# Performance work log

Measured on AMD Instinct MI355X. Metric: run time of the kernel, lower is better.

Reference implementation:

```python
import jax, jax.numpy as jnp
import numpy as np

IMC = 256
EPS = 1e-6
BN_EPS = 1e-5
GRID = (69.12, 79.36)      # (depth, width) in meters
OFF = (0.0, -39.68, 0.0)   # (xoff, yoff, zoff)
RES = 0.64
ZMIN, ZMAX = -3.0, 2.76
SCALES = [0.25, 0.125, 0.0625, 0.03125, 0.015625]


def make_corners():
    # replicates make_grid(): corner lattice in lidar coords, shape [nz, nx, ny, 3]
    nx = int(round(GRID[0] / RES)) + 1   # 109
    ny = int(round(GRID[1] / RES)) + 1   # 125
    nz = int(round((ZMAX - ZMIN) / RES)) + 1  # 10
    xc = RES * np.arange(nx) + OFF[0]
    yc = GRID[1] - RES * np.arange(ny) + OFF[1]
    zc = ZMAX - RES * np.arange(nz)
    xx, yy = np.meshgrid(xc, yc, indexing='ij')
    base = np.stack([xx, yy, np.full_like(xx, OFF[2])], axis=-1)  # [nx,ny,3]
    zoffs = np.stack([np.zeros(nz), np.zeros(nz), zc], axis=-1)   # [nz,3]
    corners = base[None] + zoffs[:, None, None, :]
    return jnp.asarray(corners, jnp.float32)


def grid_sample(img, grid):
    # img [B,C,H,W]; grid [B,P,N,2] xy in [-1,1]; bilinear, zero padding, align_corners=False
    B, C, H, W = img.shape
    x = (grid[..., 0] + 1.0) * (W * 0.5) - 0.5
    y = (grid[..., 1] + 1.0) * (H * 0.5) - 0.5
    x0f = jnp.floor(x); y0f = jnp.floor(y)
    wx = (x - x0f).reshape(B, 1, -1)
    wy = (y - y0f).reshape(B, 1, -1)
    x0 = x0f.astype(jnp.int32); y0 = y0f.astype(jnp.int32)
    flat = img.reshape(B, C, H * W)
    def g(xi, yi):
        ok = ((xi >= 0) & (xi < W) & (yi >= 0) & (yi < H)).reshape(B, 1, -1)
        idx = (jnp.clip(yi, 0, H - 1) * W + jnp.clip(xi, 0, W - 1)).reshape(B, 1, -1)
        return jnp.take_along_axis(flat, idx, axis=2) * ok
    v00 = g(x0, y0); v01 = g(x0 + 1, y0); v10 = g(x0, y0 + 1); v11 = g(x0 + 1, y0 + 1)
    out = (v00 * (1 - wx) + v01 * wx) * (1 - wy) + (v10 * (1 - wx) + v11 * wx) * wy
    return out.reshape(B, C, grid.shape[1], grid.shape[2])


def oft(feats, calib, corners, scale, w, b):
    B, C, Hf, Wf = feats.shape
    # perspective projection of grid corners into the image plane
    hom = jnp.einsum('bij,zdwj->bzdwi', calib[:, :, :3], corners) + calib[:, None, None, None, :, 3]
    xy = hom[..., :2] / hom[..., 2:3]                      # [B,nz,nx,ny,2]
    img_size = jnp.array([Wf, Hf], jnp.float32) / scale
    nc = jnp.clip(2.0 * xy / img_size - 1.0, -1.0, 1.0)
    mn = jnp.minimum(nc[:, :-1, :-1, :-1], nc[:, :-1, 1:, :-1])
    mx = jnp.maximum(nc[:, 1:, 1:, 1:], nc[:, 1:, :-1, 1:])
    bbox = jnp.concatenate([mn, mx], axis=-1)              # [B,Zc,Dc,Wc,4]
    _, Zc, Dc, Wc, _ = bbox.shape
    bbox = bbox.reshape(B, Zc, Dc * Wc, 4)
    area = ((bbox[..., 2] - bbox[..., 0]) * (bbox[..., 3] - bbox[..., 1])
            * (Hf * Wf * 0.25) + EPS)[:, None]             # [B,1,Zc,N]
    visible = (area > EPS).astype(feats.dtype)
    ii = jnp.cumsum(jnp.cumsum(feats, axis=-1), axis=-2)   # integral image
    tl = grid_sample(ii, jnp.stack([bbox[..., 0], bbox[..., 1]], -1))
    br = grid_sample(ii, jnp.stack([bbox[..., 2], bbox[..., 3]], -1))
    tr = grid_sample(ii, jnp.stack([bbox[..., 2], bbox[..., 1]], -1))
    bl = grid_sample(ii, jnp.stack([bbox[..., 0], bbox[..., 3]], -1))
    vox = (tl + br - tr - bl) / area * visible             # [B,C,Zc,N]
    vox = vox.transpose(0, 3, 1, 2).reshape(B * Dc * Wc, C * Zc)
    ortho = jax.nn.relu(vox @ w.T + b).reshape(B, Dc, Wc, -1)
    return ortho.transpose(0, 3, 2, 1)                     # [B,imc,Wc,Dc]


def attention(x, aw, ab):
    s = jax.nn.sigmoid(x.mean(axis=(2, 3)) @ aw.T + ab)
    return x * s[:, :, None, None]


def conv3x3(x, w, stride):
    return jax.lax.conv_general_dilated(x, w, (stride, stride), ((1, 1), (1, 1)),
                                        dimension_numbers=('NCHW', 'OIHW', 'NCHW'))


def bn(x, g, b, m, v):
    scale = g / jnp.sqrt(v + BN_EPS)
    return (x - m[None, :, None, None]) * scale[None, :, None, None] + b[None, :, None, None]


def make_calib(B):
    K = np.array([[560.0, 0.0, 640.0], [0.0, 560.0, 192.0], [0.0, 0.0, 1.0]])
    Rt = np.array([[0.0, -1.0, 0.0, 0.05],   # lidar(x fwd, y left, z up) -> cam(x right, y down, z fwd)
                   [0.0, 0.0, -1.0, -0.30],
                   [1.0, 0.0, 0.0, 0.27]])
    P = K @ Rt
    return jnp.asarray(np.tile(P[None], (B, 1, 1)), jnp.float32)


def setup_inputs() -> dict:
    key = jax.random.key(0)
    ks = jax.random.split(key, 16)
    B = 1
    shapes = [(B, IMC, 96, 320), (B, IMC, 48, 160), (B, IMC, 24, 80), (B, IMC, 12, 40), (B, IMC, 6, 20)]
    feats = [jax.random.normal(ks[i], s, jnp.float32) * 0.1 for i, s in enumerate(shapes)]
    HC = 9 * IMC  # height_channels = int((2.76-(-3))/0.64 * 256) = 2304
    inp = {
        'feats04': feats[0], 'feats08': feats[1], 'feats16': feats[2],
        'feats32': feats[3], 'feats64': feats[4],
        'calib': make_calib(B),
        'oft_w': jax.random.normal(ks[5], (5, IMC, HC), jnp.float32) * 0.02,
        'oft_b': jax.random.normal(ks[6], (5, IMC), jnp.float32) * 0.02,
        'att_w': jax.random.normal(ks[7], (IMC, IMC), jnp.float32) * 0.05,
        'att_b': jnp.zeros((IMC,), jnp.float32),
        'conv1_w': jax.random.normal(ks[8], (IMC, IMC * 5, 3, 3), jnp.float32) * 0.02,
        'bn1_g': 1.0 + 0.1 * jax.random.normal(ks[9], (IMC,), jnp.float32),
        'bn1_b': 0.05 * jax.random.normal(ks[10], (IMC,), jnp.float32),
        'bn1_m': 0.05 * jax.random.normal(ks[11], (IMC,), jnp.float32),
        'bn1_v': jax.random.uniform(ks[12], (IMC,), jnp.float32, 0.5, 1.5),
        'conv2_w': jax.random.normal(ks[13], (IMC, IMC, 3, 3), jnp.float32) * 0.02,
        'bn2_g': 1.0 + 0.1 * jax.random.normal(ks[14], (IMC,), jnp.float32),
        'bn2_b': jnp.zeros((IMC,), jnp.float32),
        'bn2_m': jnp.zeros((IMC,), jnp.float32),
        'bn2_v': jax.random.uniform(ks[15], (IMC,), jnp.float32, 0.5, 1.5),
    }
    return inp


def reference(feats04, feats08, feats16, feats32, feats64, calib,
              oft_w, oft_b, att_w, att_b,
              conv1_w, bn1_g, bn1_b, bn1_m, bn1_v,
              conv2_w, bn2_g, bn2_b, bn2_m, bn2_v):
    corners = make_corners()
    feats = [feats04, feats08, feats16, feats32, feats64]
    orthos = [attention(oft(f, calib, corners, s, oft_w[i], oft_b[i]), att_w, att_b)
              for i, (f, s) in enumerate(zip(feats, SCALES))]
    x = jnp.concatenate(orthos, axis=1)            # [B, 5*imc, 124, 108]
    x = jax.nn.relu(bn(conv3x3(x, conv1_w, 2), bn1_g, bn1_b, bn1_m, bn1_v))
    x = jax.nn.relu(bn(conv3x3(x, conv2_w, 1), bn2_g, bn2_b, bn2_m, bn2_v))
    return x                                       # [B, imc, 62, 54]
```

## Files before the change

### kernel.cpp

```cpp
#include <hip/hip_runtime.h>

typedef __attribute__((ext_vector_type(8))) short short8;
typedef __attribute__((ext_vector_type(4))) float float4v;
typedef __attribute__((ext_vector_type(4))) int int4v;
typedef __attribute__((ext_vector_type(4))) unsigned short ushort4v;

#define NBOX 13392
#define ZC 9
#define KOFT 2304
#define NPIX 3348
#define NBLK0 105
#define NBLKC 27
#define TILEK 4096
#define NBSTRIDE 294912
#define VOXSZ 30965760

__device__ __forceinline__ unsigned short f2bf(float f) {
  union { float f; unsigned int i; } v; v.f = f;
  unsigned int r = v.i + 0x7FFFu + ((v.i >> 16) & 1u);
  return (unsigned short)(r >> 16);
}
__device__ __forceinline__ float bf2f(unsigned short u) {
  union { unsigned int i; float f; } v; v.i = ((unsigned int)u) << 16; return v.f;
}
__device__ __forceinline__ float i2f(int i) {
  union { int i; float f; } v; v.i = i; return v.f;
}

__device__ __forceinline__ const int* uniform_ptr(const int* p) {
  unsigned lo = (unsigned)(uintptr_t)p;
  unsigned hi = (unsigned)((uintptr_t)p >> 32);
  lo = (unsigned)__builtin_amdgcn_readfirstlane((int)lo);
  hi = (unsigned)__builtin_amdgcn_readfirstlane((int)hi);
  return (const int*)(((uintptr_t)hi << 32) | (uintptr_t)lo);
}

__device__ __forceinline__ void async16(const unsigned short* g, unsigned short* l) {
  __builtin_amdgcn_global_load_lds(
      (const __attribute__((address_space(1))) unsigned int*)g,
      (__attribute__((address_space(3))) unsigned int*)l, 16, 0, 0);
}

__global__ void k_alpha_beta(const float* __restrict__ oft_b,
                             const float* __restrict__ g1, const float* __restrict__ b1,
                             const float* __restrict__ m1, const float* __restrict__ v1,
                             const float* __restrict__ g2, const float* __restrict__ b2,
                             const float* __restrict__ m2, const float* __restrict__ v2,
                             float* __restrict__ ALPHA, float* __restrict__ BETA,
                             float* __restrict__ MEANS, unsigned short* __restrict__ ZPAGE) {
  int g = blockIdx.x, c = threadIdx.x;
  float al, be;
  if (g < 5) { al = 1.f; be = oft_b[g * 256 + c]; MEANS[g * 256 + c] = 0.f; }
  else {
    const float* gg = (g == 5) ? g1 : g2;
    const float* bb = (g == 5) ? b1 : b2;
    const float* mm = (g == 5) ? m1 : m2;
    const float* vv = (g == 5) ? v1 : v2;
    al = gg[c] / sqrtf(vv[c] + 1e-5f);
    be = bb[c] - mm[c] * al;
  }
  ALPHA[g * 256 + c] = al; BETA[g * 256 + c] = be;
  if (g == 0) ZPAGE[c] = 0;
}

__global__ void k_wpermT(const float* __restrict__ w, unsigned short* __restrict__ wp) {
  int idx = blockIdx.x * 256 + threadIdx.x;
  int sc = idx / 589824;
  int r  = idx % 589824;
  int j   = r & 7;
  int row = (r >> 3) & 127;
  int kc  = (r >> 10) & 3;
  int cs  = r >> 12;
  int cb  = cs / 72, s = cs % 72;
  int oc = cb * 128 + row;
  int k  = s * 32 + kc * 8 + j;
  int z = k >> 8, c = k & 255;
  wp[idx] = f2bf(w[((size_t)sc * 256 + oc) * 2304 + c * 9 + z]);
}

__global__ void k_wperm1T(const float* __restrict__ w, const float* __restrict__ satt,
                          unsigned short* __restrict__ wp) {
  int idx = blockIdx.x * 256 + threadIdx.x;
  int j   = idx & 7;
  int row = (idx >> 3) & 127;
  int kc  = (idx >> 10) & 3;
  int rest = idx >> 12;
  int s = rest % 40; rest /= 40;
  int r = rest % 9;  int cb = rest / 9;
  int oc = cb * 128 + row;
  int ic = s * 32 + kc * 8 + j;
  wp[idx] = f2bf(w[(size_t)oc * 11520 + ic * 9 + r] * satt[ic]);
}

__global__ void k_wperm2T(const float* __restrict__ w, unsigned short* __restrict__ wp) {
  int idx = blockIdx.x * 256 + threadIdx.x;
  int j   = idx & 7;
  int row = (idx >> 3) & 127;
  int kc  = (idx >> 10) & 3;
  int rest = idx >> 12;
  int s = rest % 8; rest /= 8;
  int r = rest % 9; int cb = rest / 9;
  int oc = cb * 128 + row;
  int ic = s * 32 + kc * 8 + j;
  wp[idx] = f2bf(w[(size_t)oc * 2304 + ic * 9 + r]);
}

__global__ void k_taps(const float* __restrict__ calib, int* __restrict__ taps,
                       int Hf, int Wf, float areaScale) {
  int idx = blockIdx.x * 256 + threadIdx.x;
  if (idx >= ZC * NBOX) return;
  int z = idx / NBOX, n = idx % NBOX;
  int d = n / 124, wj = n % 124;
  float P[12];
#pragma unroll
  for (int i = 0; i < 12; ++i) P[i] = calib[i];
  auto proj = [&](int k, int i, int j, float& nxo, float& nyo) {
    float X = 0.64f * (float)i;
    float Y = 39.68f - 0.64f * (float)j;
    float Z = 2.76f - 0.64f * (float)k;
    float hx = P[0] * X + P[1] * Y + P[2]  * Z + P[3];
    float hy = P[4] * X + P[5] * Y + P[6]  * Z + P[7];
    float hz = P[8] * X + P[9] * Y + P[10] * Z + P[11];
    float px = hx / hz, py = hy / hz;
    nxo = 2.f * px / 1280.f - 1.f; nxo = fminf(fmaxf(nxo, -1.f), 1.f);
    nyo = 2.f * py / 384.f  - 1.f; nyo = fminf(fmaxf(nyo, -1.f), 1.f);
  };
  float ax, ay, bx, by, cx, cy, dx, dy;
  proj(z,     d,     wj,     ax, ay);
  proj(z,     d + 1, wj,     bx, by);
  proj(z + 1, d + 1, wj + 1, cx, cy);
  proj(z + 1, d,     wj + 1, dx, dy);
  float x0 = fminf(ax, bx), y0 = fminf(ay, by);
  float x1 = fmaxf(cx, dx), y1 = fmaxf(cy, dy);
  float rawA = (x1 - x0) * (y1 - y0) * areaScale;
  int* ob = taps + (size_t)idx * 32;
  if (!(rawA > 0.f)) { ob[0] = 0; return; }
  float inv = 1.f / (rawA + 1e-6f);

  float u0 = (x0 + 1.f) * ((float)Wf * 0.5f) - 0.5f;
  float u1 = (x1 + 1.f) * ((float)Wf * 0.5f) - 0.5f;
  float fu0 = floorf(u0), fu1 = floorf(u1);
  int cx0 = (int)fu0, cx1 = (int)fu1;
  float wx0 = u0 - fu0, wx1 = u1 - fu1;
  int xs[4]; float xw[4];
  xs[0] = cx0; xs[1] = cx0 + 1; xs[2] = cx1; xs[3] = cx1 + 1;
  xw[0] = (1.f - wx0) * inv; xw[1] = wx0 * inv;
  xw[2] = -(1.f - wx1) * inv; xw[3] = -wx1 * inv;
  int dcx = cx1 - cx0;
  if (dcx == 0)      { xw[0] += xw[2]; xw[1] += xw[3]; xw[2] = 0.f; xw[3] = 0.f; }
  else if (dcx == 1) { xw[1] += xw[2]; xw[2] = xw[3]; xs[2] = xs[3]; xw[3] = 0.f; }
#pragma unroll
  for (int j = 0; j < 4; ++j) {
    if (xs[j] < 0 || xs[j] >= Wf) xw[j] = 0.f;
    xs[j] = min(max(xs[j], 0), Wf - 1);
  }
#define CSWX(a, b) { if (xw[a] == 0.f && xw[b] != 0.f) { \
    float tw = xw[a]; xw[a] = xw[b]; xw[b] = tw; \
    int ts = xs[a]; xs[a] = xs[b]; xs[b] = ts; } }
  CSWX(0, 1) CSWX(2, 3) CSWX(0, 2) CSWX(1, 3) CSWX(1, 2)
#undef CSWX
  int nx = (xw[0] != 0.f) + (xw[1] != 0.f) + (xw[2] != 0.f) + (xw[3] != 0.f);

  float v0 = (y0 + 1.f) * ((float)Hf * 0.5f) - 0.5f;
  float v1 = (y1 + 1.f) * ((float)Hf * 0.5f) - 0.5f;
  float fv0 = floorf(v0), fv1 = floorf(v1);
  int ry0 = (int)fv0, ry1 = (int)fv1;
  float wy0 = v0 - fv0, wy1 = v1 - fv1;
  int ys[4]; float yw[4];
  ys[0] = ry0; ys[1] = ry0 + 1; ys[2] = ry1; ys[3] = ry1 + 1;
  yw[0] = 1.f - wy0; yw[1] = wy0; yw[2] = -(1.f - wy1); yw[3] = -wy1;
  int dcy = ry1 - ry0;
  if (dcy == 0)      { yw[0] += yw[2]; yw[1] += yw[3]; yw[2] = 0.f; yw[3] = 0.f; }
  else if (dcy == 1) { yw[1] += yw[2]; yw[2] = yw[3]; ys[2] = ys[3]; yw[3] = 0.f; }
#pragma unroll
  for (int j = 0; j < 4; ++j) {
    if (ys[j] < 0 || ys[j] >= Hf) yw[j] = 0.f;
    ys[j] = min(max(ys[j], 0), Hf - 1);
  }
#define CSWY(a, b) { if (yw[a] == 0.f && yw[b] != 0.f) { \
    float tw = yw[a]; yw[a] = yw[b]; yw[b] = tw; \
    int ts = ys[a]; ys[a] = ys[b]; ys[b] = ts; } }
  CSWY(0, 1) CSWY(2, 3) CSWY(0, 2) CSWY(1, 3) CSWY(1, 2)
#undef CSWY
  int ny = (yw[0] != 0.f) + (yw[1] != 0.f) + (yw[2] != 0.f) + (yw[3] != 0.f);

  if (nx == 0 || ny == 0) { ob[0] = 0; return; }

  int off[16]; float w[16];
#pragma unroll
  for (int r = 0; r < 4; ++r)
#pragma unroll
    for (int c = 0; c < 4; ++c) {
      off[r * 4 + c] = (ys[r] * Wf + xs[c]) * 1024;
      w[r * 4 + c] = yw[r] * xw[c];
    }
  off[0] |= (nx << 25) | (ny << 28);
  int4v* obv = (int4v*)ob;
#pragma unroll
  for (int i = 0; i < 4; ++i)
    obv[i] = (int4v){off[4 * i], off[4 * i + 1], off[4 * i + 2], off[4 * i + 3]};
  float4v* wb = (float4v*)obv;
#pragma unroll
  for (int i = 0; i < 4; ++i)
    wb[4 + i] = (float4v){w[4 * i], w[4 * i + 1], w[4 * i + 2], w[4 * i + 3]};
}

__global__ void k_transpose_all(const float* __restrict__ f0, const float* __restrict__ f1,
                                const float* __restrict__ f2, const float* __restrict__ f3,
                                const float* __restrict__ f4, float* __restrict__ II) {
  int b = blockIdx.x;
  int sc, cx;
  if (b < 480)      { sc = 0; cx = b; }
  else if (b < 600) { sc = 1; cx = b - 480; }
  else if (b < 630) { sc = 2; cx = b - 600; }
  else if (b < 638) { sc = 3; cx = b - 630; }
  else              { sc = 4; cx = b - 638; }
  const int Ss[5] = {30720, 7680, 1920, 480, 120};
  const size_t IIof[5] = {0, 7864320, 9830400, 10321920, 10444800};
  const float* srcs[5] = {f0, f1, f2, f3, f4};
  int S = Ss[sc];
  const float* src = srcs[sc];
  float* dst = II + IIof[sc];
  __shared__ float tile[64][65];
  int t = threadIdx.x;
  int wave = t >> 6, lane = t & 63;
  int s0 = cx * 64, c0 = blockIdx.y * 64;
#pragma unroll
  for (int i = 0; i < 16; ++i) {
    int c_l = wave * 16 + i;
    if (s0 + lane < S) tile[c_l][lane] = src[(size_t)(c0 + c_l) * S + s0 + lane];
  }
  __syncthreads();
#pragma unroll
  for (int i = 0; i < 16; ++i) {
    int s_l = wave * 16 + i;
    if (s0 + s_l < S) dst[(size_t)(s0 + s_l) * 256 + c0 + lane] = tile[lane][s_l];
  }
}

__global__ void k_cumw_all(float* __restrict__ II) {
  int b = blockIdx.x;
  int sc, h;
  if (b < 96)       { sc = 0; h = b; }
  else if (b < 144) { sc = 1; h = b - 96; }
  else if (b < 168) { sc = 2; h = b - 144; }
  else if (b < 180) { sc = 3; h = b - 168; }
  else              { sc = 4; h = b - 180; }
  const int Wfs[5] = {320, 160, 80, 40, 20};
  const size_t IIof[5] = {0, 7864320, 9830400, 10321920, 10444800};
  int Wf = Wfs[sc];
  float* p = II + IIof[sc] + (size_t)h * Wf * 256 + threadIdx.x;
  float acc = 0.f;
#pragma unroll 4
  for (int w = 0; w < Wf; ++w) { acc += p[(size_t)w * 256]; p[(size_t)w * 256] = acc; }
}

__global__ void k_cumh_all(float* __restrict__ II) {
  int b = blockIdx.x;
  int sc, w;
  if (b < 320)      { sc = 0; w = b; }
  else if (b < 480) { sc = 1; w = b - 320; }
  else if (b < 560) { sc = 2; w = b - 480; }
  else if (b < 600) { sc = 3; w = b - 560; }
  else              { sc = 4; w = b - 600; }
  const int Wfs[5] = {320, 160, 80, 40, 20};
  const int Hfs[5] = {96, 48, 24, 12, 6};
  const size_t IIof[5] = {0, 7864320, 9830400, 10321920, 10444800};
  int Hf = Hfs[sc];
  size_t stride = (size_t)Wfs[sc] * 256;
  float* p = II + IIof[sc] + (size_t)w * 256 + threadIdx.x;
  float acc = 0.f;
#pragma unroll 4
  for (int h = 0; h < Hf; ++h) { acc += p[h * stride]; p[h * stride] = acc; }
}

__global__ __launch_bounds__(512) void k_sample(const float* __restrict__ ii,
                                                const int* __restrict__ taps,
                                                unsigned short* __restrict__ voxT) {
  __shared__ unsigned short st[3][8][66][4];
  int t = threadIdx.x;
  int wave = t >> 6, lane = t & 63;
  int n = blockIdx.x * 8 + wave;
  int zg = blockIdx.y * 3;
  const char* iib = (const char*)ii + (lane << 4);
#pragma unroll
  for (int dz = 0; dz < 3; ++dz) {
    int z = zg + dz;
    const int* tb = uniform_ptr(taps + (size_t)(z * NBOX + n) * 32);
    int o_[16];
#pragma unroll
    for (int i = 0; i < 16; ++i) o_[i] = tb[i];
    unsigned h = (unsigned)o_[0];
    int nx = (h >> 25) & 7;
    int ny = (h >> 28) & 7;
    o_[0] = (int)(h & 0x01FFFFFFu);
    ushort4v o;
    if (ny == 0) {
      o[0] = 0; o[1] = 0; o[2] = 0; o[3] = 0;
    } else {
      float w_[16];
#pragma unroll
      for (int i = 0; i < 16; ++i) w_[i] = i2f(tb[16 + i]);
      float4v a0 = {0.f, 0.f, 0.f, 0.f}, a1 = a0;
#define TAP(i, acc) { float4v t_ = *(const float4v*)(iib + (size_t)(unsigned)o_[i]); acc += t_ * w_[i]; }
      TAP(0, a0)
      if (nx > 1) TAP(1, a1)
      if (nx > 2) TAP(2, a0)
      if (nx > 3) TAP(3, a1)
      if (ny > 1) {
        TAP(4, a0)
        if (nx > 1) TAP(5, a1)
        if (nx > 2) TAP(6, a0)
        if (nx > 3) TAP(7, a1)
      }
      if (ny > 2) {
        TAP(8, a0)
        if (nx > 1) TAP(9, a1)
        if (nx > 2) TAP(10, a0)
        if (nx > 3) TAP(11, a1)
      }
      if (ny > 3) {
        TAP(12, a0)
        if (nx > 1) TAP(13, a1)
        if (nx > 2) TAP(14, a0)
        if (nx > 3) TAP(15, a1)
      }
#undef TAP
      float4v acc = a0 + a1;
#pragma unroll
      for (int j = 0; j < 4; ++j) o[j] = f2bf(acc[j]);
    }
    *(ushort4v*)&st[dz][wave][lane][0] = o;
  }
  __syncthreads();
  int nb = (blockIdx.x * 8) >> 7;
  int r0 = (blockIdx.x * 8) & 127;
  unsigned short* outb = voxT + (size_t)nb * NBSTRIDE + (size_t)r0 * 32;
  int lane32 = t & 31;
  int row = lane32 >> 2, kc = lane32 & 3;
  int kcS = kc ^ ((row >> 1) & 3);
#pragma unroll
  for (int p = 0; p < 2; ++p) {
    int q = p * 16 + (t >> 5);
    if (q < 24) {
      int zq = q >> 3;
      int si = q & 7;
      short8 v = *(const short8*)&st[zq][row][si * 8 + kc * 2][0];
      *(short8*)(outb + (size_t)(zg + zq) * 32768 + (size_t)si * 4096
                 + (size_t)(row * 32 + kcS * 8)) = v;
    }
  }
}

__global__ __launch_bounds__(256) void k_gemmT_all(
    const unsigned short* __restrict__ AT, const unsigned short* __restrict__ BT,
    const float* __restrict__ beta, unsigned short* __restrict__ xbuf, int s0) {
  __shared__ unsigned short ls[8704];
  unsigned short* lsA = ls;
  unsigned short* lsB = ls + 4096;
  int t = threadIdx.x;
  int lane = t & 63, wave = t >> 6;
  int l15 = lane & 15, quad = lane >> 4;
  int nb = blockIdx.x, cb = blockIdx.y;
  int slab = blockIdx.z, sc = s0 + slab;
  int wrow = (wave >> 1) * 64, wcol = (wave & 1) * 64;
  int quadS = quad ^ ((l15 >> 1) & 3);

  const unsigned short* ga = AT + (size_t)slab * VOXSZ + (size_t)nb * NBSTRIDE + t * 8;
  const unsigned short* gb = BT + (size_t)sc * 589824 + (size_t)cb * NBSTRIDE + t * 8;
  unsigned short* ldA = lsA + t * 8;
  unsigned short* ldB = lsB + t * 8;

  float4v acc[4][4];
#pragma unroll
  for (int mi = 0; mi < 4; ++mi)
#pragma unroll
    for (int ni = 0; ni < 4; ++ni) acc[mi][ni] = (float4v){0.f, 0.f, 0.f, 0.f};

  for (int s = 0; s < 72; ++s) {
    async16(ga, ldA);
    async16(ga + 2048, ldA + 2048);
    async16(gb, ldB);
    async16(gb + 2048, ldB + 2048);
    ga += TILEK; gb += TILEK;
    __syncthreads();
    short8 af[4], bf[4];
    const short8* pA = (const short8*)lsA;
    const short8* pB = (const short8*)lsB;
#pragma unroll
    for (int mi = 0; mi < 4; ++mi) af[mi] = pA[(wrow + mi * 16 + l15) * 4 + quadS];
#pragma unroll
    for (int ni = 0; ni < 4; ++ni) bf[ni] = pB[quad * 128 + wcol + ni * 16 + l15];
#pragma unroll
    for (int mi = 0; mi < 4; ++mi)
#pragma unroll
      for (int ni = 0; ni < 4; ++ni)
        acc[mi][ni] = __builtin_amdgcn_mfma_f32_16x16x32_bf16(af[mi], bf[ni], acc[mi][ni], 0, 0, 0);
    __syncthreads();
  }

  float bval[4];
#pragma unroll
  for (int ni = 0; ni < 4; ++ni)
    bval[ni] = beta[sc * 256 + cb * 128 + wcol + ni * 16 + l15];
#pragma unroll
  for (int ph = 0; ph < 2; ++ph) {
    if (wrow == ph * 64) {
#pragma unroll
      for (int mi = 0; mi < 4; ++mi)
#pragma unroll
        for (int ni = 0; ni < 4; ++ni)
#pragma unroll
          for (int j = 0; j < 4; ++j) {
            int row = mi * 16 + quad * 4 + j;
            int col = wcol + ni * 16 + l15;
            float v = acc[mi][ni][j] + bval[ni];
            ls[row * 136 + col] = f2bf(v > 0.f ? v : 0.f);
          }
    }
    __syncthreads();
#pragma unroll
    for (int it = 0; it < 4; ++it) {
      int idx = it * 256 + t;
      int row = idx >> 4, ch = idx & 15;
      int nn = nb * 128 + ph * 64 + row;
      if (nn < NBOX) {
        short8 v = *(const short8*)&ls[row * 136 + ch * 8];
        *(short8*)(xbuf + (size_t)nn * 1280 + sc * 256 + cb * 128 + ch * 8) = v;
      }
    }
    __syncthreads();
  }
}

__global__ __launch_bounds__(256) void k_gemmT(
    const unsigned short* __restrict__ AT, const unsigned short* __restrict__ BT,
    float* __restrict__ part) {
  __shared__ unsigned short lsA[4096];
  __shared__ unsigned short lsB[4096];
  int t = threadIdx.x;
  int lane = t & 63, wave = t >> 6;
  int l15 = lane & 15, quad = lane >> 4;
  int nb = blockIdx.x, cb = blockIdx.y, ks = blockIdx.z;
  int wrow = (wave >> 1) * 64, wcol = (wave & 1) * 64;
  int quadS = quad ^ ((l15 >> 1) & 3);

  const unsigned short* ga = AT + (size_t)nb * NBSTRIDE + (size_t)ks * 18 * TILEK + t * 8;
  const unsigned short* gb = BT + (size_t)cb * NBSTRIDE + (size_t)ks * 18 * TILEK + t * 8;
  unsigned short* ldA = lsA + t * 8;
  unsigned short* ldB = lsB + t * 8;

  float4v acc[4][4];
#pragma unroll
  for (int mi = 0; mi < 4; ++mi)
#pragma unroll
    for (int ni = 0; ni < 4; ++ni) acc[mi][ni] = (float4v){0.f, 0.f, 0.f, 0.f};

  for (int s = 0; s < 18; ++s) {
    async16(ga, ldA);
    async16(ga + 2048, ldA + 2048);
    async16(gb, ldB);
    async16(gb + 2048, ldB + 2048);
    ga += TILEK; gb += TILEK;
    __syncthreads();
    short8 af[4], bf[4];
    const short8* pA = (const short8*)lsA;
    const short8* pB = (const short8*)lsB;
#pragma unroll
    for (int mi = 0; mi < 4; ++mi) af[mi] = pA[(wrow + mi * 16 + l15) * 4 + quadS];
#pragma unroll
    for (int ni = 0; ni < 4; ++ni) bf[ni] = pB[quad * 128 + wcol + ni * 16 + l15];
#pragma unroll
    for (int mi = 0; mi < 4; ++mi)
#pragma unroll
      for (int ni = 0; ni < 4; ++ni)
        acc[mi][ni] = __builtin_amdgcn_mfma_f32_16x16x32_bf16(af[mi], bf[ni], acc[mi][ni], 0, 0, 0);
    __syncthreads();
  }

#pragma unroll
  for (int mi = 0; mi < 4; ++mi) {
    int nb0 = nb * 128 + wrow + mi * 16 + quad * 4;
#pragma unroll
    for (int j = 0; j < 4; ++j) {
      int nn = nb0 + j;
      if (nn < NBOX) {
#pragma unroll
        for (int ni = 0; ni < 4; ++ni) {
          int oc = cb * 128 + wcol + ni * 16 + l15;
          part[((size_t)ks * NBOX + nn) * 256 + oc] = acc[mi][ni][j];
        }
      }
    }
  }
}

__global__ void k_redoft(const float* __restrict__ part, const float* __restrict__ beta,
                         unsigned short* __restrict__ xbuf, int choff) {
  int n = blockIdx.x, oc = threadIdx.x;
  float v = part[(size_t)n * 256 + oc]
          + part[((size_t)NBOX + n) * 256 + oc]
          + part[((size_t)2 * NBOX + n) * 256 + oc]
          + part[((size_t)3 * NBOX + n) * 256 + oc];
  v += beta[oc];
  v = v > 0.f ? v : 0.f;
  xbuf[(size_t)n * 1280 + choff + oc] = f2bf(v);
}

template <int MODE>
__global__ __launch_bounds__(256) void k_gemmS(
    const unsigned short* __restrict__ A, const unsigned short* __restrict__ BT,
    float* __restrict__ part, const unsigned short* __restrict__ zpage) {
  constexpr int KIC   = (MODE == 1) ? 1280 : 256;
  constexpr int STEPS = KIC / 32;
  __shared__ unsigned short lsA[4096];
  __shared__ unsigned short lsB[4096];
  int t = threadIdx.x;
  int lane = t & 63, wave = t >> 6;
  int l15 = lane & 15, quad = lane >> 4;
  int n0 = blockIdx.x * 128, oc0 = blockIdx.y * 128;
  int r = blockIdx.z;
  int wrow = (wave >> 1) * 64, wcol = (wave & 1) * 64;
  int srow = t & 127, skc = t >> 7;

  int p = n0 + srow;
  int oy = p / 54, ox = p - oy * 54;
  int ky = r / 3, kx = r - ky * 3;
  bool valid; int sp;
  if (MODE == 1) {
    int ih = 2 * oy + ky - 1, iw = 2 * ox + kx - 1;
    valid = (p < NPIX) && ((unsigned)ih < 124u) && ((unsigned)iw < 108u);
    sp = iw * 124 + ih;
  } else {
    int ih = oy + ky - 1, iw = ox + kx - 1;
    valid = (p < NPIX) && ((unsigned)ih < 62u) && ((unsigned)iw < 54u);
    sp = ih * 54 + iw;
  }
  const unsigned short* ga = valid ? (A + (size_t)sp * KIC + skc * 8) : zpage;
  int astep = valid ? 32 : 0;
  const unsigned short* gb = BT + ((size_t)(blockIdx.y * 9 + r) * STEPS) * TILEK + t * 8;
  unsigned short* ldA = lsA + t * 8;
  unsigned short* ldB = lsB + t * 8;

  float4v acc[4][4];
#pragma unroll
  for (int mi = 0; mi < 4; ++mi)
#pragma unroll
    for (int ni = 0; ni < 4; ++ni) acc[mi][ni] = (float4v){0.f, 0.f, 0.f, 0.f};

  for (int s = 0; s < STEPS; ++s) {
    async16(ga, ldA);
    async16(ga + 16, ldA + 2048);
    async16(gb, ldB);
    async16(gb + 2048, ldB + 2048);
    ga += astep; gb += TILEK;
    __syncthreads();
    short8 af[4], bf[4];
    const short8* pA = (const short8*)lsA;
    const short8* pB = (const short8*)lsB;
#pragma unroll
    for (int mi = 0; mi < 4; ++mi) af[mi] = pA[quad * 128 + wrow + mi * 16 + l15];
#pragma unroll
    for (int ni = 0; ni < 4; ++ni) bf[ni] = pB[quad * 128 + wcol + ni * 16 + l15];
#pragma unroll
    for (int mi = 0; mi < 4; ++mi)
#pragma unroll
      for (int ni = 0; ni < 4; ++ni)
        acc[mi][ni] = __builtin_amdgcn_mfma_f32_16x16x32_bf16(af[mi], bf[ni], acc[mi][ni], 0, 0, 0);
    __syncthreads();
  }

#pragma unroll
  for (int mi = 0; mi < 4; ++mi) {
    int nb0 = n0 + wrow + mi * 16 + quad * 4;
#pragma unroll
    for (int j = 0; j < 4; ++j) {
      int nn = nb0 + j;
      if (nn < NPIX) {
#pragma unroll
        for (int ni = 0; ni < 4; ++ni) {
          int oc = oc0 + wcol + ni * 16 + l15;
          part[((size_t)r * NPIX + nn) * 256 + oc] = acc[mi][ni][j];
        }
      }
    }
  }
}

template <bool F32OUT>
__global__ void k_redconv(const float* __restrict__ part, const float* __restrict__ alpha,
                          const float* __restrict__ beta, void* __restrict__ outv) {
  int p = blockIdx.x, oc = threadIdx.x;
  float v = 0.f;
#pragma unroll
  for (int r = 0; r < 9; ++r) v += part[((size_t)r * NPIX + p) * 256 + oc];
  v = v * alpha[oc] + beta[oc];
  v = v > 0.f ? v : 0.f;
  if (F32OUT) ((float*)outv)[(size_t)oc * NPIX + p] = v;
  else ((unsigned short*)outv)[(size_t)p * 256 + oc] = f2bf(v);
}

__global__ void k_means2(const unsigned short* __restrict__ x, float* __restrict__ means) {
  int tid = threadIdx.x;
  if (tid >= 160) return;
  int c0 = tid * 8;
  int r0 = blockIdx.x * 64;
  float part[8] = {0.f, 0.f, 0.f, 0.f, 0.f, 0.f, 0.f, 0.f};
  for (int i = 0; i < 64; ++i) {
    int row = r0 + i;
    if (row < NBOX) {
      short8 v = *(const short8*)(x + (size_t)row * 1280 + c0);
#pragma unroll
      for (int j = 0; j < 8; ++j) part[j] += bf2f((unsigned short)v[j]);
    }
  }
#pragma unroll
  for (int j = 0; j < 8; ++j) atomicAdd(&means[c0 + j], part[j]);
}

__global__ void k_att(const float* __restrict__ means, const float* __restrict__ aw,
                      const float* __restrict__ ab, float* __restrict__ satt) {
  int sc = blockIdx.x, c = threadIdx.x;
  __shared__ float m[256];
  m[c] = means[sc * 256 + c] * (1.f / (float)NBOX);
  __syncthreads();
  float acc = ab[c];
  for (int j = 0; j < 256; ++j) acc += m[j] * aw[c * 256 + j];
  satt[sc * 256 + c] = 1.f / (1.f + expf(-acc));
}

extern "C" void kernel_launch(void* const* d_in, const int* in_sizes, int n_in,
                              void* d_out, int out_size, void* d_ws, size_t ws_size,
                              hipStream_t stream) {
  const float* feats[5];
  for (int i = 0; i < 5; ++i) feats[i] = (const float*)d_in[i];
  const float* calib   = (const float*)d_in[5];
  const float* oft_w   = (const float*)d_in[6];
  const float* oft_b   = (const float*)d_in[7];
  const float* att_w   = (const float*)d_in[8];
  const float* att_b   = (const float*)d_in[9];
  const float* conv1_w = (const float*)d_in[10];
  const float* bn1g = (const float*)d_in[11];
  const float* bn1b = (const float*)d_in[12];
  const float* bn1m = (const float*)d_in[13];
  const float* bn1v = (const float*)d_in[14];
  const float* conv2_w = (const float*)d_in[15];
  const float* bn2g = (const float*)d_in[16];
  const float* bn2b = (const float*)d_in[17];
  const float* bn2m = (const float*)d_in[18];
  const float* bn2v = (const float*)d_in[19];

  char* ws = (char*)d_ws;
  size_t off = 0;
  auto alloc = [&](size_t bytes) -> void* {
    void* p = ws + off; off += (bytes + 255) & ~(size_t)255; return p;
  };
  unsigned short* WPERMT = (unsigned short*)alloc((size_t)5 * 589824 * 2);
  unsigned short* WC1T   = (unsigned short*)alloc((size_t)2949120 * 2);
  unsigned short* WC2T   = (unsigned short*)alloc((size_t)589824 * 2);
  float*          II     = (float*)alloc((size_t)10475520 * 4);
  unsigned short* XBUF   = (unsigned short*)alloc((size_t)NBOX * 1280 * 2);
  unsigned short* Y1     = (unsigned short*)alloc((size_t)NPIX * 256 * 2);
  float*          MEANS  = (float*)alloc(1280 * 4);
  float*          SATT   = (float*)alloc(1280 * 4);
  float*          ALPHA  = (float*)alloc(7 * 256 * 4);
  float*          BETA   = (float*)alloc(7 * 256 * 4);
  unsigned short* ZPAGE  = (unsigned short*)alloc(256 * 2);

  const size_t SLAB   = (size_t)VOXSZ * 2;
  const size_t TAPSZ  = (size_t)ZC * NBOX * 128;
  const size_t PARTSZ = (size_t)4 * NBOX * 256 * 4;
  size_t rem = (ws_size > off) ? ws_size - off : 0;

  int NS;
  int* TAPS; unsigned short* VOXT; float* PART;
  if (rem >= 5 * SLAB) {
    NS = 5;
    VOXT = (unsigned short*)alloc(5 * SLAB);
    TAPS = (int*)XBUF;
    PART = (float*)VOXT;
  } else if (rem >= 2 * SLAB + TAPSZ) {
    NS = (int)((rem - TAPSZ) / SLAB); if (NS > 4) NS = 4;
    TAPS = (int*)alloc(TAPSZ);
    VOXT = (unsigned short*)alloc((size_t)NS * SLAB);
    PART = (float*)VOXT;
  } else {
    NS = 0;
    VOXT = (unsigned short*)alloc(SLAB);
    PART = (float*)alloc(PARTSZ);
    TAPS = (int*)PART;
  }
  (void)in_sizes; (void)n_in; (void)out_size;

  static const int HFs[5] = {96, 48, 24, 12, 6};
  static const int WFs[5] = {320, 160, 80, 40, 20};
  static const size_t IIoff[5] = {0, 7864320, 9830400, 10321920, 10444800};

  k_alpha_beta<<<7, 256, 0, stream>>>(oft_b, bn1g, bn1b, bn1m, bn1v,
                                      bn2g, bn2b, bn2m, bn2v, ALPHA, BETA, MEANS, ZPAGE);
  k_wpermT<<<11520, 256, 0, stream>>>(oft_w, WPERMT);
  k_wperm2T<<<2304, 256, 0, stream>>>(conv2_w, WC2T);

  k_transpose_all<<<dim3(640, 4), 256, 0, stream>>>(feats[0], feats[1], feats[2],
                                                    feats[3], feats[4], II);
  k_cumw_all<<<186, 256, 0, stream>>>(II);
  k_cumh_all<<<620, 256, 0, stream>>>(II);

  if (NS > 0) {
    int g0 = 0;
    while (g0 < 5) {
      int gsz = 5 - g0; if (gsz > NS) gsz = NS;
      for (int s = g0; s < g0 + gsz; ++s) {
        k_taps<<<(ZC * NBOX + 255) / 256, 256, 0, stream>>>(
            calib, TAPS, HFs[s], WFs[s], (float)(HFs[s] * WFs[s]) * 0.25f);
        k_sample<<<dim3(NBOX / 8, 3), 512, 0, stream>>>(
            II + IIoff[s], TAPS, VOXT + (size_t)(s - g0) * VOXSZ);
      }
      k_gemmT_all<<<dim3(NBLK0, 2, gsz), 256, 0, stream>>>(VOXT, WPERMT, BETA, XBUF, g0);
      g0 += gsz;
    }
  } else {
    for (int s = 0; s < 5; ++s) {
      k_taps<<<(ZC * NBOX + 255) / 256, 256, 0, stream>>>(
          calib, TAPS, HFs[s], WFs[s], (float)(HFs[s] * WFs[s]) * 0.25f);
      k_sample<<<dim3(NBOX / 8, 3), 512, 0, stream>>>(II + IIoff[s], TAPS, VOXT);
      k_gemmT<<<dim3(NBLK0, 2, 4), 256, 0, stream>>>(
          VOXT, WPERMT + (size_t)s * 589824, PART);
      k_redoft<<<NBOX, 256, 0, stream>>>(PART, BETA + s * 256, XBUF, s * 256);
    }
  }

  k_means2<<<(NBOX + 63) / 64, 256, 0, stream>>>(XBUF, MEANS);
  k_att<<<5, 256, 0, stream>>>(MEANS, att_w, att_b, SATT);
  k_wperm1T<<<11520, 256, 0, stream>>>(conv1_w, SATT, WC1T);

  k_gemmS<1><<<dim3(NBLKC, 2, 9), 256, 0, stream>>>(XBUF, WC1T, PART, ZPAGE);
  k_redconv<false><<<NPIX, 256, 0, stream>>>(PART, ALPHA + 5 * 256, BETA + 5 * 256, Y1);

  k_gemmS<2><<<dim3(NBLKC, 2, 9), 256, 0, stream>>>(Y1, WC2T, PART, ZPAGE);
  k_redconv<true><<<NPIX, 256, 0, stream>>>(PART, ALPHA + 6 * 256, BETA + 6 * 256, d_out);
}
```

Before: 878.3 us.

## Store separable tap offsets/weights, batch taps+sample across scales, drop LDS swizzle

Tap records now hold 4 x-offsets, 4 y-offsets and 4 x/y weights (16 ints instead of 32), and the sampler builds the 16 bilinear offset/weight products itself. Tap generation and sampling for all scales in a group are launched as single kernels via a grid z/y dimension, with per-scale sizes kept in constant memory. This cuts tap memory traffic and launch count. The XOR swizzle on the A-operand LDS layout is removed from both the sample writer and the GEMM readers, which simplifies indexing but may bring back LDS bank conflicts.

```diff
diff --git a/kernel.cpp b/kernel.cpp
--- a/kernel.cpp
+++ b/kernel.cpp
@@ -14,6 +14,7 @@
 #define TILEK 4096
 #define NBSTRIDE 294912
 #define VOXSZ 30965760
+#define TAPINTS 16
 
 __device__ __forceinline__ unsigned short f2bf(float f) {
   union { float f; unsigned int i; } v; v.f = f;
@@ -26,6 +27,10 @@
 __device__ __forceinline__ float i2f(int i) {
   union { int i; float f; } v; v.i = i; return v.f;
 }
+
+__device__ __constant__ int cHFs[5] = {96, 48, 24, 12, 6};
+__device__ __constant__ int cWFs[5] = {320, 160, 80, 40, 20};
+__device__ __constant__ size_t cIIof[5] = {0, 7864320, 9830400, 10321920, 10444800};
 
 __device__ __forceinline__ const int* uniform_ptr(const int* p) {
   unsigned lo = (unsigned)(uintptr_t)p;
@@ -105,10 +110,12 @@
   wp[idx] = f2bf(w[(size_t)oc * 2304 + ic * 9 + r]);
 }
 
-__global__ void k_taps(const float* __restrict__ calib, int* __restrict__ taps,
-                       int Hf, int Wf, float areaScale) {
+__global__ void k_tapsA(const float* __restrict__ calib, int* __restrict__ taps, int s0) {
   int idx = blockIdx.x * 256 + threadIdx.x;
   if (idx >= ZC * NBOX) return;
+  int slab = blockIdx.y, sc = s0 + slab;
+  int Hf = cHFs[sc], Wf = cWFs[sc];
+  float areaScale = (float)(Hf * Wf) * 0.25f;
   int z = idx / NBOX, n = idx % NBOX;
   int d = n / 124, wj = n % 124;
   float P[12];
@@ -133,7 +140,7 @@
   float x0 = fminf(ax, bx), y0 = fminf(ay, by);
   float x1 = fmaxf(cx, dx), y1 = fmaxf(cy, dy);
   float rawA = (x1 - x0) * (y1 - y0) * areaScale;
-  int* ob = taps + (size_t)idx * 32;
+  int* ob = taps + (size_t)slab * (ZC * NBOX * TAPINTS) + (size_t)idx * TAPINTS;
   if (!(rawA > 0.f)) { ob[0] = 0; return; }
   float inv = 1.f / (rawA + 1e-6f);
 
@@ -186,23 +193,14 @@
 
   if (nx == 0 || ny == 0) { ob[0] = 0; return; }
 
-  int off[16]; float w[16];
-#pragma unroll
-  for (int r = 0; r < 4; ++r)
-#pragma unroll
-    for (int c = 0; c < 4; ++c) {
-      off[r * 4 + c] = (ys[r] * Wf + xs[c]) * 1024;
-      w[r * 4 + c] = yw[r] * xw[c];
-    }
-  off[0] |= (nx << 25) | (ny << 28);
   int4v* obv = (int4v*)ob;
-#pragma unroll
-  for (int i = 0; i < 4; ++i)
-    obv[i] = (int4v){off[4 * i], off[4 * i + 1], off[4 * i + 2], off[4 * i + 3]};
-  float4v* wb = (float4v*)obv;
-#pragma unroll
-  for (int i = 0; i < 4; ++i)
-    wb[4 + i] = (float4v){w[4 * i], w[4 * i + 1], w[4 * i + 2], w[4 * i + 3]};
+  obv[0] = (int4v){(xs[0] << 10) | (nx << 25) | (ny << 28),
+                   xs[1] << 10, xs[2] << 10, xs[3] << 10};
+  obv[1] = (int4v){ys[0] * Wf * 1024, ys[1] * Wf * 1024,
+                   ys[2] * Wf * 1024, ys[3] * Wf * 1024};
+  float4v* wb = (float4v*)ob;
+  wb[2] = (float4v){xw[0], xw[1], xw[2], xw[3]};
+  wb[3] = (float4v){yw[0], yw[1], yw[2], yw[3]};
 }
 
 __global__ void k_transpose_all(const float* __restrict__ f0, const float* __restrict__ f1,
@@ -216,11 +214,10 @@
   else if (b < 638) { sc = 3; cx = b - 630; }
   else              { sc = 4; cx = b - 638; }
   const int Ss[5] = {30720, 7680, 1920, 480, 120};
-  const size_t IIof[5] = {0, 7864320, 9830400, 10321920, 10444800};
   const float* srcs[5] = {f0, f1, f2, f3, f4};
   int S = Ss[sc];
   const float* src = srcs[sc];
-  float* dst = II + IIof[sc];
+  float* dst = II + cIIof[sc];
   __shared__ float tile[64][65];
   int t = threadIdx.x;
   int wave = t >> 6, lane = t & 63;
@@ -246,10 +243,8 @@
   else if (b < 168) { sc = 2; h = b - 144; }
   else if (b < 180) { sc = 3; h = b - 168; }
   else              { sc = 4; h = b - 180; }
-  const int Wfs[5] = {320, 160, 80, 40, 20};
-  const size_t IIof[5] = {0, 7864320, 9830400, 10321920, 10444800};
-  int Wf = Wfs[sc];
-  float* p = II + IIof[sc] + (size_t)h * Wf * 256 + threadIdx.x;
+  int Wf = cWFs[sc];
+  float* p = II + cIIof[sc] + (size_t)h * Wf * 256 + threadIdx.x;
   float acc = 0.f;
 #pragma unroll 4
   for (int w = 0; w < Wf; ++w) { acc += p[(size_t)w * 256]; p[(size_t)w * 256] = acc; }
@@ -263,44 +258,58 @@
   else if (b < 560) { sc = 2; w = b - 480; }
   else if (b < 600) { sc = 3; w = b - 560; }
   else              { sc = 4; w = b - 600; }
-  const int Wfs[5] = {320, 160, 80, 40, 20};
   const int Hfs[5] = {96, 48, 24, 12, 6};
-  const size_t IIof[5] = {0, 7864320, 9830400, 10321920, 10444800};
   int Hf = Hfs[sc];
-  size_t stride = (size_t)Wfs[sc] * 256;
-  float* p = II + IIof[sc] + (size_t)w * 256 + threadIdx.x;
+  size_t stride = (size_t)cWFs[sc] * 256;
+  float* p = II + cIIof[sc] + (size_t)w * 256 + threadIdx.x;
   float acc = 0.f;
 #pragma unroll 4
   for (int h = 0; h < Hf; ++h) { acc += p[h * stride]; p[h * stride] = acc; }
 }
 
-__global__ __launch_bounds__(512) void k_sample(const float* __restrict__ ii,
-                                                const int* __restrict__ taps,
-                                                unsigned short* __restrict__ voxT) {
+__global__ __launch_bounds__(512) void k_sampleA(const float* __restrict__ II,
+                                                 const int* __restrict__ taps,
+                                                 unsigned short* __restrict__ voxT,
+                                                 int s0) {
   __shared__ unsigned short st[3][8][66][4];
   int t = threadIdx.x;
   int wave = t >> 6, lane = t & 63;
   int n = blockIdx.x * 8 + wave;
   int zg = blockIdx.y * 3;
+  int slab = blockIdx.z, sc = s0 + slab;
+  const float* ii = II + cIIof[sc];
+  const int* tbase = taps + (size_t)slab * (ZC * NBOX * TAPINTS);
+  unsigned short* vox = voxT + (size_t)slab * VOXSZ;
   const char* iib = (const char*)ii + (lane << 4);
 #pragma unroll
   for (int dz = 0; dz < 3; ++dz) {
     int z = zg + dz;
-    const int* tb = uniform_ptr(taps + (size_t)(z * NBOX + n) * 32);
-    int o_[16];
-#pragma unroll
-    for (int i = 0; i < 16; ++i) o_[i] = tb[i];
-    unsigned h = (unsigned)o_[0];
+    const int* tb = uniform_ptr(tbase + (size_t)(z * NBOX + n) * TAPINTS);
+    int xo[4], yo[4]; float xw[4], yw[4];
+#pragma unroll
+    for (int i = 0; i < 4; ++i) xo[i] = tb[i];
+#pragma unroll
+    for (int i = 0; i < 4; ++i) yo[i] = tb[4 + i];
+#pragma unroll
+    for (int i = 0; i < 4; ++i) xw[i] = i2f(tb[8 + i]);
+#pragma unroll
+    for (int i = 0; i < 4; ++i) yw[i] = i2f(tb[12 + i]);
+    unsigned h = (unsigned)xo[0];
     int nx = (h >> 25) & 7;
     int ny = (h >> 28) & 7;
-    o_[0] = (int)(h & 0x01FFFFFFu);
+    xo[0] = (int)(h & 0x01FFFFFFu);
     ushort4v o;
     if (ny == 0) {
       o[0] = 0; o[1] = 0; o[2] = 0; o[3] = 0;
     } else {
-      float w_[16];
-#pragma unroll
-      for (int i = 0; i < 16; ++i) w_[i] = i2f(tb[16 + i]);
+      int o_[16]; float w_[16];
+#pragma unroll
+      for (int r = 0; r < 4; ++r)
+#pragma unroll
+        for (int c = 0; c < 4; ++c) {
+          o_[r * 4 + c] = yo[r] + xo[c];
+          w_[r * 4 + c] = yw[r] * xw[c];
+        }
       float4v a0 = {0.f, 0.f, 0.f, 0.f}, a1 = a0;
 #define TAP(i, acc) { float4v t_ = *(const float4v*)(iib + (size_t)(unsigned)o_[i]); acc += t_ * w_[i]; }
       TAP(0, a0)
@@ -335,10 +344,9 @@
   __syncthreads();
   int nb = (blockIdx.x * 8) >> 7;
   int r0 = (blockIdx.x * 8) & 127;
-  unsigned short* outb = voxT + (size_t)nb * NBSTRIDE + (size_t)r0 * 32;
+  unsigned short* outb = vox + (size_t)nb * NBSTRIDE + (size_t)r0 * 32;
   int lane32 = t & 31;
   int row = lane32 >> 2, kc = lane32 & 3;
-  int kcS = kc ^ ((row >> 1) & 3);
 #pragma unroll
   for (int p = 0; p < 2; ++p) {
     int q = p * 16 + (t >> 5);
@@ -347,7 +355,7 @@
       int si = q & 7;
       short8 v = *(const short8*)&st[zq][row][si * 8 + kc * 2][0];
       *(short8*)(outb + (size_t)(zg + zq) * 32768 + (size_t)si * 4096
-                 + (size_t)(row * 32 + kcS * 8)) = v;
+                 + (size_t)(row * 32 + kc * 8)) = v;
     }
   }
 }
@@ -364,7 +372,6 @@
   int nb = blockIdx.x, cb = blockIdx.y;
   int slab = blockIdx.z, sc = s0 + slab;
   int wrow = (wave >> 1) * 64, wcol = (wave & 1) * 64;
-  int quadS = quad ^ ((l15 >> 1) & 3);
 
   const unsigned short* ga = AT + (size_t)slab * VOXSZ + (size_t)nb * NBSTRIDE + t * 8;
   const unsigned short* gb = BT + (size_t)sc * 589824 + (size_t)cb * NBSTRIDE + t * 8;
@@ -388,7 +395,7 @@
     const short8* pA = (const short8*)lsA;
     const short8* pB = (const short8*)lsB;
 #pragma unroll
-    for (int mi = 0; mi < 4; ++mi) af[mi] = pA[(wrow + mi * 16 + l15) * 4 + quadS];
+    for (int mi = 0; mi < 4; ++mi) af[mi] = pA[(wrow + mi * 16 + l15) * 4 + quad];
 #pragma unroll
     for (int ni = 0; ni < 4; ++ni) bf[ni] = pB[quad * 128 + wcol + ni * 16 + l15];
 #pragma unroll
@@ -443,7 +450,6 @@
   int l15 = lane & 15, quad = lane >> 4;
   int nb = blockIdx.x, cb = blockIdx.y, ks = blockIdx.z;
   int wrow = (wave >> 1) * 64, wcol = (wave & 1) * 64;
-  int quadS = quad ^ ((l15 >> 1) & 3);
 
   const unsigned short* ga = AT + (size_t)nb * NBSTRIDE + (size_t)ks * 18 * TILEK + t * 8;
   const unsigned short* gb = BT + (size_t)cb * NBSTRIDE + (size_t)ks * 18 * TILEK + t * 8;
@@ -467,7 +473,7 @@
     const short8* pA = (const short8*)lsA;
     const short8* pB = (const short8*)lsB;
 #pragma unroll
-    for (int mi = 0; mi < 4; ++mi) af[mi] = pA[(wrow + mi * 16 + l15) * 4 + quadS];
+    for (int mi = 0; mi < 4; ++mi) af[mi] = pA[(wrow + mi * 16 + l15) * 4 + quad];
 #pragma unroll
     for (int ni = 0; ni < 4; ++ni) bf[ni] = pB[quad * 128 + wcol + ni * 16 + l15];
 #pragma unroll
@@ -667,21 +673,16 @@
   float*          BETA   = (float*)alloc(7 * 256 * 4);
   unsigned short* ZPAGE  = (unsigned short*)alloc(256 * 2);
 
-  const size_t SLAB   = (size_t)VOXSZ * 2;
-  const size_t TAPSZ  = (size_t)ZC * NBOX * 128;
-  const size_t PARTSZ = (size_t)4 * NBOX * 256 * 4;
+  const size_t SLAB    = (size_t)VOXSZ * 2;
+  const size_t TAPSZ_C = (size_t)ZC * NBOX * 64;
+  const size_t PARTSZ  = (size_t)4 * NBOX * 256 * 4;
   size_t rem = (ws_size > off) ? ws_size - off : 0;
 
   int NS;
   int* TAPS; unsigned short* VOXT; float* PART;
-  if (rem >= 5 * SLAB) {
-    NS = 5;
-    VOXT = (unsigned short*)alloc(5 * SLAB);
-    TAPS = (int*)XBUF;
-    PART = (float*)VOXT;
-  } else if (rem >= 2 * SLAB + TAPSZ) {
-    NS = (int)((rem - TAPSZ) / SLAB); if (NS > 4) NS = 4;
-    TAPS = (int*)alloc(TAPSZ);
+  if (rem >= 2 * (SLAB + TAPSZ_C)) {
+    NS = (int)(rem / (SLAB + TAPSZ_C)); if (NS > 5) NS = 5;
+    TAPS = (int*)alloc((size_t)NS * TAPSZ_C);
     VOXT = (unsigned short*)alloc((size_t)NS * SLAB);
     PART = (float*)VOXT;
   } else {
@@ -692,10 +693,6 @@
   }
   (void)in_sizes; (void)n_in; (void)out_size;
 
-  static const int HFs[5] = {96, 48, 24, 12, 6};
-  static const int WFs[5] = {320, 160, 80, 40, 20};
-  static const size_t IIoff[5] = {0, 7864320, 9830400, 10321920, 10444800};
-
   k_alpha_beta<<<7, 256, 0, stream>>>(oft_b, bn1g, bn1b, bn1m, bn1v,
                                       bn2g, bn2b, bn2m, bn2v, ALPHA, BETA, MEANS, ZPAGE);
   k_wpermT<<<11520, 256, 0, stream>>>(oft_w, WPERMT);
@@ -706,24 +703,20 @@
   k_cumw_all<<<186, 256, 0, stream>>>(II);
   k_cumh_all<<<620, 256, 0, stream>>>(II);
 
+  const int TGRID = (ZC * NBOX + 255) / 256;
   if (NS > 0) {
     int g0 = 0;
     while (g0 < 5) {
       int gsz = 5 - g0; if (gsz > NS) gsz = NS;
-      for (int s = g0; s < g0 + gsz; ++s) {
-        k_taps<<<(ZC * NBOX + 255) / 256, 256, 0, stream>>>(
-            calib, TAPS, HFs[s], WFs[s], (float)(HFs[s] * WFs[s]) * 0.25f);
-        k_sample<<<dim3(NBOX / 8, 3), 512, 0, stream>>>(
-            II + IIoff[s], TAPS, VOXT + (size_t)(s - g0) * VOXSZ);
-      }
+      k_tapsA<<<dim3(TGRID, gsz), 256, 0, stream>>>(calib, TAPS, g0);
+      k_sampleA<<<dim3(NBOX / 8, 3, gsz), 512, 0, stream>>>(II, TAPS, VOXT, g0);
       k_gemmT_all<<<dim3(NBLK0, 2, gsz), 256, 0, stream>>>(VOXT, WPERMT, BETA, XBUF, g0);
       g0 += gsz;
     }
   } else {
     for (int s = 0; s < 5; ++s) {
-      k_taps<<<(ZC * NBOX + 255) / 256, 256, 0, stream>>>(
-          calib, TAPS, HFs[s], WFs[s], (float)(HFs[s] * WFs[s]) * 0.25f);
-      k_sample<<<dim3(NBOX / 8, 3), 512, 0, stream>>>(II + IIoff[s], TAPS, VOXT);
+      k_tapsA<<<dim3(TGRID, 1), 256, 0, stream>>>(calib, TAPS, s);
+      k_sampleA<<<dim3(NBOX / 8, 3, 1), 512, 0, stream>>>(II, TAPS, VOXT, s);
       k_gemmT<<<dim3(NBLK0, 2, 4), 256, 0, stream>>>(
           VOXT, WPERMT + (size_t)s * 589824, PART);
       k_redoft<<<NBOX, 256, 0, stream>>>(PART, BETA + s * 256, XBUF, s * 256);
```

After: 797.1 us. -9.2%, faster.
